# Performance work log

Measured on AMD Instinct MI355X. Metric: run time of the kernel, lower is better.

Reference implementation:

```python
import jax, jax.numpy as jnp
import numpy as np

N_SCALES = 5
EPS = 1e-8


def setup_inputs() -> dict:
    key = jax.random.key(0)
    # [B, T] log-return series
    log_returns = jax.random.normal(key, (4096, 8192), dtype=jnp.float32) * 0.01
    return {"log_returns": log_returns}


def _log_rs(x, s):
    """Mean over chunks of the R/S statistic at scale s, in log space.

    x: [B, T] -> returns [B].  Vectorizes the per-chunk loop of the torch
    module by reshaping to [B, n_chunks, s].
    """
    B, T = x.shape
    nc = T // s
    chunks = x[:, : nc * s].reshape(B, nc, s)
    y = chunks - chunks.mean(axis=-1, keepdims=True)
    cs = jnp.cumsum(y, axis=-1)
    R = cs.max(axis=-1) - cs.min(axis=-1)                 # [B, nc]
    S = jnp.maximum(jnp.std(chunks, axis=-1, ddof=1), EPS)  # unbiased std, clamp(min=1e-8)
    rs = jnp.maximum(R / S, EPS)
    return jnp.log(jnp.maximum(rs.mean(axis=-1), EPS))    # [B]


def reference(log_returns):
    x = log_returns
    B, T = x.shape
    # scale schedule is a pure function of the static length T
    min_scale = max(4, T // 2 ** N_SCALES)
    scales = []
    for k in range(N_SCALES):
        s = max(4, min_scale * 2 ** k)
        if s > T // 2:
            break
        scales.append(s)
    # log-log OLS slope: H = Cov(log n, log R/S) / Var(log n)
    ln = jnp.log(jnp.array(scales, dtype=x.dtype))                     # [K]
    lr = jnp.stack([_log_rs(x, s) for s in scales], axis=-1)           # [B, K]
    ln_c = ln - ln.mean()
    lr_c = lr - lr.mean(axis=-1, keepdims=True)
    num = (ln_c * lr_c).sum(axis=-1)
    den = jnp.maximum((ln_c ** 2).sum(), 1e-8)
    return jnp.clip(num / den, 0.05, 0.95)                             # [B]
```

## Files before the change

kernel.cpp:

```cpp
#include <hip/hip_runtime.h>
#include <math.h>

#define TLEN 8192
#define HALF 4096
#define NTH  256

__device__ __forceinline__ int padi(int i) { return i + (i >> 5); }

__global__ __launch_bounds__(NTH) void hurst_kernel(const float* __restrict__ x,
                                                    float* __restrict__ out) {
    __shared__ float SB[HALF + (HALF >> 5)];
    __shared__ float Sp[513];
    __shared__ float SSp[513];
    __shared__ float wsum[4], wssq[4];
    __shared__ float meanL[62], SL[62];
    __shared__ float pmax[72], pmin[72];
    __shared__ float rsb[62];

    const int t = threadIdx.x;
    const int lane = t & 63;
    const int wave = t >> 6;
    const float* xr = x + (long long)blockIdx.x * TLEN;

    float P[2][16];
    float carry_s = 0.f, carry_q = 0.f;

    #pragma unroll
    for (int h = 0; h < 2; ++h) {
        const float* xh = xr + h * HALF;
        #pragma unroll
        for (int j = 0; j < 4; ++j) {
            int p = j * 1024 + t * 4;
            float4 v = *reinterpret_cast<const float4*>(xh + p);
            SB[padi(p)]     = v.x;
            SB[padi(p + 1)] = v.y;
            SB[padi(p + 2)] = v.z;
            SB[padi(p + 3)] = v.w;
        }
        __syncthreads();

        const int base = 16 * t + (t >> 1);
        float rr[16];
        float ssum = 0.f, ssq = 0.f;
        #pragma unroll
        for (int k = 0; k < 16; ++k) {
            float v = SB[base + k];
            rr[k] = v;
            ssum += v;
            ssq = fmaf(v, v, ssq);
        }

        float v1 = ssum, v2 = ssq;
        #pragma unroll
        for (int d = 1; d < 64; d <<= 1) {
            float u1 = __shfl_up(v1, d, 64);
            float u2 = __shfl_up(v2, d, 64);
            if (lane >= d) { v1 += u1; v2 += u2; }
        }
        if (lane == 63) { wsum[wave] = v1; wssq[wave] = v2; }
        __syncthreads();
        float w0 = wsum[0], w1 = wsum[1], w2 = wsum[2], w3 = wsum[3];
        float q0 = wssq[0], q1 = wssq[1], q2 = wssq[2], q3 = wssq[3];
        float woff1 = carry_s, woff2 = carry_q;
        if (wave > 0) { woff1 += w0; woff2 += q0; }
        if (wave > 1) { woff1 += w1; woff2 += q1; }
        if (wave > 2) { woff1 += w2; woff2 += q2; }
        carry_s += w0 + w1 + w2 + w3;
        carry_q += q0 + q1 + q2 + q3;

        float ex1 = woff1 + (v1 - ssum);
        float ex2 = woff2 + (v2 - ssq);
        Sp[h * 256 + t]  = ex1;
        SSp[h * 256 + t] = ex2;

        float run = ex1;
        #pragma unroll
        for (int k = 0; k < 16; ++k) { run += rr[k]; P[h][k] = run; }
    }
    if (t == 0) { Sp[512] = carry_s; SSp[512] = carry_q; }
    __syncthreads();

    if (t < 62) {
        int si, ci;
        if (t < 32)      { si = 0; ci = t; }
        else if (t < 48) { si = 1; ci = t - 32; }
        else if (t < 56) { si = 2; ci = t - 48; }
        else if (t < 60) { si = 3; ci = t - 56; }
        else             { si = 4; ci = t - 60; }
        int g = 16 << si;
        int a = ci * g, b = a + g;
        float s_f = (float)(256 << si);
        float sum = Sp[b] - Sp[a];
        float sq  = SSp[b] - SSp[a];
        float m = sum / s_f;
        float var = (sq - s_f * m * m) / (s_f - 1.0f);
        meanL[t] = m;
        SL[t] = fmaxf(sqrtf(fmaxf(var, 0.f)), 1e-8f);
    }
    __syncthreads();

    #pragma unroll
    for (int si = 0; si < 5; ++si) {
        const int lg = 4 + si;
        const int g = 1 << lg;
        const int OFF  = (si == 0) ? 0 : (si == 1) ? 32 : (si == 2) ? 48 : (si == 3) ? 56 : 60;
        const int POFF = (si == 0) ? 0 : (si == 1) ? 32 : (si == 2) ? 48 : (si == 3) ? 56 : 64;
        const int c0 = t >> lg;
        const int c1 = (256 >> lg) + c0;
        const float m0 = meanL[OFF + c0];
        const float m1 = meanL[OFF + c1];

        float mx0 = -INFINITY, mn0 = INFINITY, mx1 = -INFINITY, mn1 = INFINITY;
        #pragma unroll
        for (int k = 0; k < 16; ++k) {
            float g0 = fmaf(-m0, (float)k, P[0][k]);
            float g1 = fmaf(-m1, (float)k, P[1][k]);
            mx0 = fmaxf(mx0, g0); mn0 = fminf(mn0, g0);
            mx1 = fmaxf(mx1, g1); mn1 = fminf(mn1, g1);
        }
        const float rb1 = (float)(16 * (t & (g - 1)) + 1);
        mx0 -= rb1 * m0; mn0 -= rb1 * m0;
        mx1 -= rb1 * m1; mn1 -= rb1 * m1;

        const int bw = (g < 64) ? g : 64;
        #pragma unroll
        for (int w = 1; w < bw; w <<= 1) {
            mx0 = fmaxf(mx0, __shfl_xor(mx0, w, 64));
            mn0 = fminf(mn0, __shfl_xor(mn0, w, 64));
            mx1 = fmaxf(mx1, __shfl_xor(mx1, w, 64));
            mn1 = fminf(mn1, __shfl_xor(mn1, w, 64));
        }
        if ((t & (bw - 1)) == 0) {
            const int pc  = (g > 64) ? (g >> 6) : 1;
            const int sub = (t >> 6) & (pc - 1);
            pmax[POFF + c0 * pc + sub] = mx0;
            pmin[POFF + c0 * pc + sub] = mn0;
            pmax[POFF + c1 * pc + sub] = mx1;
            pmin[POFF + c1 * pc + sub] = mn1;
        }
    }
    __syncthreads();

    if (t < 62) {
        int si, ci;
        if (t < 32)      { si = 0; ci = t; }
        else if (t < 48) { si = 1; ci = t - 32; }
        else if (t < 56) { si = 2; ci = t - 48; }
        else if (t < 60) { si = 3; ci = t - 56; }
        else             { si = 4; ci = t - 60; }
        const int pc   = (si == 3) ? 2 : (si == 4) ? 4 : 1;
        const int POFF = (si == 0) ? 0 : (si == 1) ? 32 : (si == 2) ? 48 : (si == 3) ? 56 : 64;
        int bsl = POFF + ci * pc;
        float mx = pmax[bsl], mn = pmin[bsl];
        #pragma unroll 4
        for (int j = 1; j < pc; ++j) {
            mx = fmaxf(mx, pmax[bsl + j]);
            mn = fminf(mn, pmin[bsl + j]);
        }
        float R = mx - mn;
        rsb[t] = fmaxf(R / SL[t], 1e-8f);
    }
    __syncthreads();

    float lrv = 0.f;
    if (t < 5) {
        const int nc  = 32 >> t;
        const int OFF = (t == 0) ? 0 : (t == 1) ? 32 : (t == 2) ? 48 : (t == 3) ? 56 : 60;
        float s = 0.f;
        for (int j = 0; j < nc; ++j) s += rsb[OFF + j];
        lrv = logf(fmaxf(s / (float)nc, 1e-8f));
    }
    if (wave == 0) {
        float n0 = __shfl(lrv, 0, 64);
        float n1 = __shfl(lrv, 1, 64);
        float n3 = __shfl(lrv, 3, 64);
        float n4 = __shfl(lrv, 4, 64);
        if (lane == 0) {
            float H = (-2.f * n0 - n1 + n3 + 2.f * n4)
                      * (1.0f / (10.0f * 0.69314718055994530942f));
            H = fminf(fmaxf(H, 0.05f), 0.95f);
            out[blockIdx.x] = H;
        }
    }
}

extern "C" void kernel_launch(void* const* d_in, const int* in_sizes, int n_in,
                              void* d_out, int out_size, void* d_ws, size_t ws_size,
                              hipStream_t stream) {
    const float* x = (const float*)d_in[0];
    float* out = (float*)d_out;
    const int B = in_sizes[0] / TLEN;
    hurst_kernel<<<dim3(B), dim3(NTH), 0, stream>>>(x, out);
}
```

Measured before the change: 191.7 us.

## Load row directly into registers, drop LDS staging and halved scan

Each thread now loads 32 contiguous floats straight from global memory with float4 loads and computes its local prefix sums in registers, removing the 16 KB shared-memory staging buffer and the two-half scan with carries. The chunk range reduction now works on 32 elements per thread, with one reduction per scale instead of two, and writes the R/S values directly for the smaller scales. Launch bounds ask for 4 blocks per CU. The cost is that each lane's loads now stride 128 bytes apart, so global loads are less coalesced per instruction, and register pressure rises from holding 32 floats plus 8 float4s per thread.

```diff
diff --git a/kernel.cpp b/kernel.cpp
--- a/kernel.cpp
+++ b/kernel.cpp
@@ -2,82 +2,60 @@
 #include <math.h>
 
 #define TLEN 8192
-#define HALF 4096
 #define NTH  256
 
-__device__ __forceinline__ int padi(int i) { return i + (i >> 5); }
-
-__global__ __launch_bounds__(NTH) void hurst_kernel(const float* __restrict__ x,
-                                                    float* __restrict__ out) {
-    __shared__ float SB[HALF + (HALF >> 5)];
-    __shared__ float Sp[513];
-    __shared__ float SSp[513];
+__global__ __launch_bounds__(NTH, 4) void hurst_kernel(const float* __restrict__ x,
+                                                       float* __restrict__ out) {
     __shared__ float wsum[4], wssq[4];
+    __shared__ float Sp8[33], SSp8[33];
     __shared__ float meanL[62], SL[62];
-    __shared__ float pmax[72], pmin[72];
+    __shared__ float pmax[4], pmin[4];
     __shared__ float rsb[62];
 
     const int t = threadIdx.x;
     const int lane = t & 63;
     const int wave = t >> 6;
     const float* xr = x + (long long)blockIdx.x * TLEN;
+    const float4* xq = reinterpret_cast<const float4*>(xr);
 
-    float P[2][16];
-    float carry_s = 0.f, carry_q = 0.f;
+    float4 v[8];
+    #pragma unroll
+    for (int j = 0; j < 8; ++j) v[j] = xq[8 * t + j];
+
+    float L[32];
+    float run = 0.f, ssq = 0.f;
+    #pragma unroll
+    for (int j = 0; j < 8; ++j) {
+        float a0 = v[j].x, a1 = v[j].y, a2 = v[j].z, a3 = v[j].w;
+        run += a0; L[4*j+0] = run; ssq = fmaf(a0, a0, ssq);
+        run += a1; L[4*j+1] = run; ssq = fmaf(a1, a1, ssq);
+        run += a2; L[4*j+2] = run; ssq = fmaf(a2, a2, ssq);
+        run += a3; L[4*j+3] = run; ssq = fmaf(a3, a3, ssq);
+    }
+    const float ssum = run;
+
+    float v1 = ssum, v2 = ssq;
+    #pragma unroll
+    for (int d = 1; d < 64; d <<= 1) {
+        float u1 = __shfl_up(v1, d, 64);
+        float u2 = __shfl_up(v2, d, 64);
+        if (lane >= d) { v1 += u1; v2 += u2; }
+    }
+    if (lane == 63) { wsum[wave] = v1; wssq[wave] = v2; }
+    __syncthreads();
+
+    float woff1 = 0.f, woff2 = 0.f;
+    if (wave > 0) { woff1 += wsum[0]; woff2 += wssq[0]; }
+    if (wave > 1) { woff1 += wsum[1]; woff2 += wssq[1]; }
+    if (wave > 2) { woff1 += wsum[2]; woff2 += wssq[2]; }
+    const float ex1 = woff1 + (v1 - ssum);
+    const float ex2 = woff2 + (v2 - ssq);
+
+    if ((t & 7) == 0) { Sp8[t >> 3] = ex1; SSp8[t >> 3] = ex2; }
+    if (t == NTH - 1) { Sp8[32] = ex1 + ssum; SSp8[32] = ex2 + ssq; }
 
     #pragma unroll
-    for (int h = 0; h < 2; ++h) {
-        const float* xh = xr + h * HALF;
-        #pragma unroll
-        for (int j = 0; j < 4; ++j) {
-            int p = j * 1024 + t * 4;
-            float4 v = *reinterpret_cast<const float4*>(xh + p);
-            SB[padi(p)]     = v.x;
-            SB[padi(p + 1)] = v.y;
-            SB[padi(p + 2)] = v.z;
-            SB[padi(p + 3)] = v.w;
-        }
-        __syncthreads();
-
-        const int base = 16 * t + (t >> 1);
-        float rr[16];
-        float ssum = 0.f, ssq = 0.f;
-        #pragma unroll
-        for (int k = 0; k < 16; ++k) {
-            float v = SB[base + k];
-            rr[k] = v;
-            ssum += v;
-            ssq = fmaf(v, v, ssq);
-        }
-
-        float v1 = ssum, v2 = ssq;
-        #pragma unroll
-        for (int d = 1; d < 64; d <<= 1) {
-            float u1 = __shfl_up(v1, d, 64);
-            float u2 = __shfl_up(v2, d, 64);
-            if (lane >= d) { v1 += u1; v2 += u2; }
-        }
-        if (lane == 63) { wsum[wave] = v1; wssq[wave] = v2; }
-        __syncthreads();
-        float w0 = wsum[0], w1 = wsum[1], w2 = wsum[2], w3 = wsum[3];
-        float q0 = wssq[0], q1 = wssq[1], q2 = wssq[2], q3 = wssq[3];
-        float woff1 = carry_s, woff2 = carry_q;
-        if (wave > 0) { woff1 += w0; woff2 += q0; }
-        if (wave > 1) { woff1 += w1; woff2 += q1; }
-        if (wave > 2) { woff1 += w2; woff2 += q2; }
-        carry_s += w0 + w1 + w2 + w3;
-        carry_q += q0 + q1 + q2 + q3;
-
-        float ex1 = woff1 + (v1 - ssum);
-        float ex2 = woff2 + (v2 - ssq);
-        Sp[h * 256 + t]  = ex1;
-        SSp[h * 256 + t] = ex2;
-
-        float run = ex1;
-        #pragma unroll
-        for (int k = 0; k < 16; ++k) { run += rr[k]; P[h][k] = run; }
-    }
-    if (t == 0) { Sp[512] = carry_s; SSp[512] = carry_q; }
+    for (int k = 0; k < 32; ++k) L[k] += ex1;
     __syncthreads();
 
     if (t < 62) {
@@ -87,11 +65,10 @@
         else if (t < 56) { si = 2; ci = t - 48; }
         else if (t < 60) { si = 3; ci = t - 56; }
         else             { si = 4; ci = t - 60; }
-        int g = 16 << si;
-        int a = ci * g, b = a + g;
+        int a = ci << si, b = (ci + 1) << si;
         float s_f = (float)(256 << si);
-        float sum = Sp[b] - Sp[a];
-        float sq  = SSp[b] - SSp[a];
+        float sum = Sp8[b] - Sp8[a];
+        float sq  = SSp8[b] - SSp8[a];
         float m = sum / s_f;
         float var = (sq - s_f * m * m) / (s_f - 1.0f);
         meanL[t] = m;
@@ -101,71 +78,51 @@
 
     #pragma unroll
     for (int si = 0; si < 5; ++si) {
-        const int lg = 4 + si;
-        const int g = 1 << lg;
-        const int OFF  = (si == 0) ? 0 : (si == 1) ? 32 : (si == 2) ? 48 : (si == 3) ? 56 : 60;
-        const int POFF = (si == 0) ? 0 : (si == 1) ? 32 : (si == 2) ? 48 : (si == 3) ? 56 : 64;
-        const int c0 = t >> lg;
-        const int c1 = (256 >> lg) + c0;
-        const float m0 = meanL[OFF + c0];
-        const float m1 = meanL[OFF + c1];
-
-        float mx0 = -INFINITY, mn0 = INFINITY, mx1 = -INFINITY, mn1 = INFINITY;
+        const int lg = 3 + si;
+        const int g = 8 << si;
+        const int OFF = (si == 0) ? 0 : (si == 1) ? 32 : (si == 2) ? 48
+                      : (si == 3) ? 56 : 60;
+        const int c = t >> lg;
+        const float m = meanL[OFF + c];
+        const int rel = t & (g - 1);
+        float acc = (float)(32 * rel + 1) * m;
+        float hmax = -INFINITY, hmin = INFINITY;
         #pragma unroll
-        for (int k = 0; k < 16; ++k) {
-            float g0 = fmaf(-m0, (float)k, P[0][k]);
-            float g1 = fmaf(-m1, (float)k, P[1][k]);
-            mx0 = fmaxf(mx0, g0); mn0 = fminf(mn0, g0);
-            mx1 = fmaxf(mx1, g1); mn1 = fminf(mn1, g1);
+        for (int k = 0; k < 32; ++k) {
+            float h = L[k] - acc;
+            acc += m;
+            hmax = fmaxf(hmax, h);
+            hmin = fminf(hmin, h);
         }
-        const float rb1 = (float)(16 * (t & (g - 1)) + 1);
-        mx0 -= rb1 * m0; mn0 -= rb1 * m0;
-        mx1 -= rb1 * m1; mn1 -= rb1 * m1;
-
         const int bw = (g < 64) ? g : 64;
         #pragma unroll
         for (int w = 1; w < bw; w <<= 1) {
-            mx0 = fmaxf(mx0, __shfl_xor(mx0, w, 64));
-            mn0 = fminf(mn0, __shfl_xor(mn0, w, 64));
-            mx1 = fmaxf(mx1, __shfl_xor(mx1, w, 64));
-            mn1 = fminf(mn1, __shfl_xor(mn1, w, 64));
+            hmax = fmaxf(hmax, __shfl_xor(hmax, w, 64));
+            hmin = fminf(hmin, __shfl_xor(hmin, w, 64));
         }
-        if ((t & (bw - 1)) == 0) {
-            const int pc  = (g > 64) ? (g >> 6) : 1;
-            const int sub = (t >> 6) & (pc - 1);
-            pmax[POFF + c0 * pc + sub] = mx0;
-            pmin[POFF + c0 * pc + sub] = mn0;
-            pmax[POFF + c1 * pc + sub] = mx1;
-            pmin[POFF + c1 * pc + sub] = mn1;
+        if (si < 4) {
+            if (rel == 0) {
+                float R = hmax - hmin;
+                rsb[OFF + c] = fmaxf(R / SL[OFF + c], 1e-8f);
+            }
+        } else {
+            if (lane == 0) { pmax[wave] = hmax; pmin[wave] = hmin; }
         }
     }
     __syncthreads();
 
-    if (t < 62) {
-        int si, ci;
-        if (t < 32)      { si = 0; ci = t; }
-        else if (t < 48) { si = 1; ci = t - 32; }
-        else if (t < 56) { si = 2; ci = t - 48; }
-        else if (t < 60) { si = 3; ci = t - 56; }
-        else             { si = 4; ci = t - 60; }
-        const int pc   = (si == 3) ? 2 : (si == 4) ? 4 : 1;
-        const int POFF = (si == 0) ? 0 : (si == 1) ? 32 : (si == 2) ? 48 : (si == 3) ? 56 : 64;
-        int bsl = POFF + ci * pc;
-        float mx = pmax[bsl], mn = pmin[bsl];
-        #pragma unroll 4
-        for (int j = 1; j < pc; ++j) {
-            mx = fmaxf(mx, pmax[bsl + j]);
-            mn = fminf(mn, pmin[bsl + j]);
-        }
-        float R = mx - mn;
-        rsb[t] = fmaxf(R / SL[t], 1e-8f);
+    if (t < 2) {
+        float mx = fmaxf(pmax[2 * t], pmax[2 * t + 1]);
+        float mn = fminf(pmin[2 * t], pmin[2 * t + 1]);
+        rsb[60 + t] = fmaxf((mx - mn) / SL[60 + t], 1e-8f);
     }
     __syncthreads();
 
     float lrv = 0.f;
     if (t < 5) {
         const int nc  = 32 >> t;
-        const int OFF = (t == 0) ? 0 : (t == 1) ? 32 : (t == 2) ? 48 : (t == 3) ? 56 : 60;
+        const int OFF = (t == 0) ? 0 : (t == 1) ? 32 : (t == 2) ? 48
+                      : (t == 3) ? 56 : 60;
         float s = 0.f;
         for (int j = 0; j < nc; ++j) s += rsb[OFF + j];
         lrv = logf(fmaxf(s / (float)nc, 1e-8f));
```

Result: faster. 187.9 us (-2.0%).
